# Optimization experiments

Hardware: AMD Instinct MI355X
Metric: run time of the kernel (lower is better)

## Reference

```python
import jax, jax.numpy as jnp
import numpy as np

B, C, P, D = 4096, 1000, 10, 256
N = C * P            # total prototypes
E = 160000           # edges among prototypes
MARGIN = -0.1
LOSS_WEIGHT = 0.1
EPS = 1e-12          # F.normalize eps


def _gcn_conv(x, src, dst, deg_isqrt, w, b):
    # PyG GCNConv: symmetric-normalized aggregation with self-loops (added by caller)
    xw = x @ w                                   # [N, D]
    norm = deg_isqrt[src] * deg_isqrt[dst]       # [E+N]
    msg = norm[:, None] * xw[src]                # [E+N, D]
    out = jax.ops.segment_sum(msg, dst, num_segments=N)
    return out + b


def setup_inputs() -> dict:
    key = jax.random.key(0)
    ks = jax.random.split(key, 8)
    return {
        "hidden": jax.random.normal(ks[0], (B, D), jnp.float32),
        "labels": jax.random.randint(ks[1], (B,), 0, C),
        "edge_index": jax.random.randint(ks[2], (2, E), 0, N),
        "node_features": 0.02 * jax.random.normal(ks[3], (N, D), jnp.float32),
        "w1": jax.random.normal(ks[4], (D, D), jnp.float32) / np.sqrt(D),
        "b1": jnp.zeros((D,), jnp.float32),
        "w2": jax.random.normal(ks[5], (D, D), jnp.float32) / np.sqrt(D),
        "b2": jnp.zeros((D,), jnp.float32),
    }


def reference(hidden, labels, edge_index, node_features, w1, b1, w2, b2):
    # --- PrototypeGCN over the prototype graph (self-loops + sym norm) ---
    loops = jnp.arange(N, dtype=edge_index.dtype)
    src = jnp.concatenate([edge_index[0], loops])
    dst = jnp.concatenate([edge_index[1], loops])
    deg = jax.ops.segment_sum(jnp.ones_like(dst, jnp.float32), dst, num_segments=N)
    deg_isqrt = jnp.where(deg > 0, jax.lax.rsqrt(jnp.maximum(deg, 1.0)), 0.0)
    x = node_features
    x = jax.nn.relu(_gcn_conv(x, src, dst, deg_isqrt, w1, b1))
    x = jax.nn.relu(_gcn_conv(x, src, dst, deg_isqrt, w2, b2))

    # --- cosine similarity, per-class max over prototypes ---
    hidden_norm = hidden / jnp.maximum(jnp.linalg.norm(hidden, axis=1, keepdims=True), EPS)
    proto_norm = x / jnp.maximum(jnp.linalg.norm(x, axis=1, keepdims=True), EPS)
    sim = (1.0 + hidden_norm @ proto_norm.T) / 2.0          # [B, N]
    sim_pc = sim.reshape(B, C, P)
    output = sim_pc.max(axis=2)                              # [B, C]
    topk_idx = sim_pc.argmax(axis=2)                         # [B, C]

    # --- margin-masked cross entropy ---
    ar = jnp.arange(B)
    true_scores = output[ar, labels]
    pred_labels = output.argmax(axis=1)
    pred_scores = output.max(axis=1)
    mask = (true_scores - pred_scores) > MARGIN              # [B] bool
    cnt = mask.sum()
    per_ce = -jax.nn.log_softmax(output, axis=1)[ar, labels]
    ce_loss = jnp.sum(per_ce * mask) / jnp.maximum(cnt, 1).astype(per_ce.dtype)

    # dispersion = -mean(proto_norm @ proto_norm.T) = -||sum_i p_i||^2 / N^2
    s = proto_norm.sum(axis=0)
    dispersion_loss = -(s @ s) / (N * N)
    total_loss = jnp.where(cnt == 0, 0.0, ce_loss + LOSS_WEIGHT * dispersion_loss)

    # --- vectorized usage scatter (replaces Python double loop) ---
    pos_ids = labels * P + topk_idx[ar, labels]
    positive_usage = jnp.zeros((N,), jnp.float32).at[pos_ids].add(1.0)
    wrong = (pred_labels != labels).astype(jnp.float32)
    neg_ids = pred_labels * P + topk_idx[ar, pred_labels]
    negative_usage = jnp.zeros((N,), jnp.float32).at[neg_ids].add(wrong)

    return (output, total_loss, positive_usage, negative_usage)
```

## Files before the change

### kernel.cpp

```cpp
#include <hip/hip_runtime.h>
#include <math.h>

#define B_  4096
#define C_  1000
#define P_  10
#define D_  256
#define N_  10000
#define E_  160000

typedef __attribute__((ext_vector_type(8))) short short8;
typedef __attribute__((ext_vector_type(4))) float floatx4;

#define MFMA16(a, b, c) __builtin_amdgcn_mfma_f32_16x16x32_bf16((a), (b), (c), 0, 0, 0)

__device__ __forceinline__ float waveReduceSum(float v){
  #pragma unroll
  for (int o = 32; o > 0; o >>= 1) v += __shfl_xor(v, o);
  return v;
}
__device__ __forceinline__ unsigned short f2bf(float f){
  unsigned int u = __float_as_uint(f);
  unsigned int r = (u + 0x7FFFu + ((u >> 16) & 1u)) >> 16;
  return (unsigned short)r;
}
__device__ __forceinline__ float bf2f(unsigned short b){
  return __uint_as_float(((unsigned int)b) << 16);
}
__device__ __forceinline__ void gload_lds16(const void* g, void* l){
  __builtin_amdgcn_global_load_lds((const __attribute__((address_space(1))) void*)g,
                                   (__attribute__((address_space(3))) void*)l, 16, 0, 0);
}

__global__ void k_prep(const int* __restrict__ src, const int* __restrict__ dst,
                       int* __restrict__ cursor, int* __restrict__ csr_src,
                       const float* __restrict__ w1, const float* __restrict__ w2,
                       unsigned short* __restrict__ w1h, unsigned short* __restrict__ w1l,
                       unsigned short* __restrict__ w2h, unsigned short* __restrict__ w2l,
                       float* __restrict__ zero_zone,
                       const float* __restrict__ nodef,
                       unsigned short* __restrict__ NFh, unsigned short* __restrict__ NFl,
                       const float* __restrict__ hidden,
                       unsigned short* __restrict__ HNh, unsigned short* __restrict__ HNl){
  int b = blockIdx.x;
  int t = threadIdx.x;
  if (b < 625){
    int e = b * 256 + t;
    if (e < E_){
      int d = dst[e];
      int p = atomicAdd(&cursor[d], 1);
      p = (p < 63) ? p : 63;
      csr_src[d * 64 + p] = src[e];
    }
  } else if (b < 1137){
    int bb = b - 625;
    const float* w = (bb < 256) ? w1 : w2;
    int n = bb & 255;
    float x = w[(size_t)t * 256 + n];
    unsigned short h = f2bf(x);
    unsigned short l = f2bf(x - bf2f(h));
    if (bb < 256){ w1h[(size_t)n * 256 + t] = h; w1l[(size_t)n * 256 + t] = l; }
    else         { w2h[(size_t)n * 256 + t] = h; w2l[(size_t)n * 256 + t] = l; }
  } else if (b < 1216){
    int i = (b - 1137) * 256 + t;
    if (i < 1 + 2 * N_) zero_zone[i] = 0.f;
  } else if (b < 11216){
    size_t i = (size_t)(b - 1216) * 256 + t;
    float x = nodef[i];
    unsigned short h = f2bf(x);
    NFh[i] = h;
    NFl[i] = f2bf(x - bf2f(h));
  } else {
    int r = b - 11216;
    float v = hidden[(size_t)r * 256 + t];
    float ss = waveReduceSum(v * v);
    __shared__ float red[4];
    int w = t >> 6;
    if ((t & 63) == 0) red[w] = ss;
    __syncthreads();
    float tot = red[0] + red[1] + red[2] + red[3];
    float nrm = fmaxf(sqrtf(tot), 1e-12f);
    float x = v / nrm;
    unsigned short h = f2bf(x);
    HNh[(size_t)r * 256 + t] = h;
    HNl[(size_t)r * 256 + t] = f2bf(x - bf2f(h));
  }
}

__global__ __launch_bounds__(64) void k_gemm_mfma(
    const unsigned short* __restrict__ Ah, const unsigned short* __restrict__ Al,
    const unsigned short* __restrict__ Wh, const unsigned short* __restrict__ Wl,
    float* __restrict__ outp){
  int lane = threadIdx.x;
  int l15 = lane & 15, lq = lane >> 4;
  int rb = blockIdx.x * 64;
  int nb = blockIdx.y * 32;

  floatx4 acc[4][2];
  #pragma unroll
  for (int mt = 0; mt < 4; ++mt)
    #pragma unroll
    for (int nt = 0; nt < 2; ++nt) acc[mt][nt] = (floatx4){0.f,0.f,0.f,0.f};

  int arow[4];
  #pragma unroll
  for (int mt = 0; mt < 4; ++mt){
    int r = rb + mt * 16 + l15;
    arow[mt] = (r < N_) ? r : (N_ - 1);
  }
  for (int kc = 0; kc < 256; kc += 32){
    short8 ah[4], al[4], bh[2], bl[2];
    #pragma unroll
    for (int mt = 0; mt < 4; ++mt){
      size_t o = (size_t)arow[mt] * 256 + kc + lq * 8;
      ah[mt] = *(const short8*)(Ah + o);
      al[mt] = *(const short8*)(Al + o);
    }
    #pragma unroll
    for (int nt = 0; nt < 2; ++nt){
      size_t o = (size_t)(nb + nt * 16 + l15) * 256 + kc + lq * 8;
      bh[nt] = *(const short8*)(Wh + o);
      bl[nt] = *(const short8*)(Wl + o);
    }
    #pragma unroll
    for (int nt = 0; nt < 2; ++nt)
      #pragma unroll
      for (int mt = 0; mt < 4; ++mt) acc[mt][nt] = MFMA16(al[mt], bh[nt], acc[mt][nt]);
    #pragma unroll
    for (int nt = 0; nt < 2; ++nt)
      #pragma unroll
      for (int mt = 0; mt < 4; ++mt) acc[mt][nt] = MFMA16(ah[mt], bl[nt], acc[mt][nt]);
    #pragma unroll
    for (int nt = 0; nt < 2; ++nt)
      #pragma unroll
      for (int mt = 0; mt < 4; ++mt) acc[mt][nt] = MFMA16(ah[mt], bh[nt], acc[mt][nt]);
  }
  #pragma unroll
  for (int mt = 0; mt < 4; ++mt)
    #pragma unroll
    for (int r = 0; r < 4; ++r){
      int row = rb + mt * 16 + lq * 4 + r;
      if (row < N_){
        #pragma unroll
        for (int nt = 0; nt < 2; ++nt)
          outp[(size_t)row * 256 + nb + nt * 16 + l15] = acc[mt][nt][r];
      }
    }
}

__global__ void k_agg_split(const float* __restrict__ XW, const int* __restrict__ deg,
                            const int* __restrict__ csr_src,
                            const float* __restrict__ bias,
                            unsigned short* __restrict__ Xh, unsigned short* __restrict__ Xl){
  int n    = blockIdx.x * 4 + (threadIdx.x >> 6);
  int lane = threadIdx.x & 63;
  int c4   = lane * 4;
  int dgn = deg[n];
  int dg = (dgn < 64) ? dgn : 64;
  int   esr = (lane < dg) ? csr_src[n * 64 + lane] : 0;
  float is  = 1.0f / sqrtf((float)(dgn + 1));
  float en  = (1.0f / sqrtf((float)(deg[esr] + 1))) * is;
  float4 s = *(const float4*)(XW + (size_t)n * 256 + c4);
  float w = is * is;
  float4 a = make_float4(w * s.x, w * s.y, w * s.z, w * s.w);
  float4 a2 = make_float4(0.f, 0.f, 0.f, 0.f);
  int i = 0;
  for (; i + 7 < dg; i += 8){
    int   si[8]; float ni[8];
    #pragma unroll
    for (int j = 0; j < 8; ++j){ si[j] = __shfl(esr, i+j); ni[j] = __shfl(en, i+j); }
    float4 vv[8];
    #pragma unroll
    for (int j = 0; j < 8; ++j) vv[j] = *(const float4*)(XW + (size_t)si[j] * 256 + c4);
    #pragma unroll
    for (int j = 0; j < 4; ++j){
      a.x  += ni[j]   * vv[j].x;   a.y  += ni[j]   * vv[j].y;
      a.z  += ni[j]   * vv[j].z;   a.w  += ni[j]   * vv[j].w;
      a2.x += ni[j+4] * vv[j+4].x; a2.y += ni[j+4] * vv[j+4].y;
      a2.z += ni[j+4] * vv[j+4].z; a2.w += ni[j+4] * vv[j+4].w;
    }
  }
  for (; i < dg; ++i){
    int s0 = __shfl(esr, i); float n0 = __shfl(en, i);
    float4 v0 = *(const float4*)(XW + (size_t)s0 * 256 + c4);
    a.x += n0 * v0.x; a.y += n0 * v0.y; a.z += n0 * v0.z; a.w += n0 * v0.w;
  }
  a.x += a2.x; a.y += a2.y; a.z += a2.z; a.w += a2.w;
  float4 b = *(const float4*)(bias + c4);
  float x0 = fmaxf(a.x + b.x, 0.f), x1 = fmaxf(a.y + b.y, 0.f);
  float x2 = fmaxf(a.z + b.z, 0.f), x3 = fmaxf(a.w + b.w, 0.f);
  unsigned short h0 = f2bf(x0), h1 = f2bf(x1), h2 = f2bf(x2), h3 = f2bf(x3);
  ushort4 hv = make_ushort4(h0, h1, h2, h3);
  ushort4 lv = make_ushort4(f2bf(x0 - bf2f(h0)), f2bf(x1 - bf2f(h1)),
                            f2bf(x2 - bf2f(h2)), f2bf(x3 - bf2f(h3)));
  *(ushort4*)(Xh + (size_t)n * 256 + c4) = hv;
  *(ushort4*)(Xl + (size_t)n * 256 + c4) = lv;
}

__global__ void k_agg_norm_split(const float* __restrict__ XW, const int* __restrict__ deg,
                                 const int* __restrict__ csr_src,
                                 const float* __restrict__ bias,
                                 unsigned short* __restrict__ Ph, unsigned short* __restrict__ Pl){
  int n    = blockIdx.x * 4 + (threadIdx.x >> 6);
  int lane = threadIdx.x & 63;
  int c4   = lane * 4;
  int dgn = deg[n];
  int dg = (dgn < 64) ? dgn : 64;
  int   esr = (lane < dg) ? csr_src[n * 64 + lane] : 0;
  float is  = 1.0f / sqrtf((float)(dgn + 1));
  float en  = (1.0f / sqrtf((float)(deg[esr] + 1))) * is;
  float4 s = *(const float4*)(XW + (size_t)n * 256 + c4);
  float w = is * is;
  float4 a = make_float4(w * s.x, w * s.y, w * s.z, w * s.w);
  float4 a2 = make_float4(0.f, 0.f, 0.f, 0.f);
  int i = 0;
  for (; i + 7 < dg; i += 8){
    int   si[8]; float ni[8];
    #pragma unroll
    for (int j = 0; j < 8; ++j){ si[j] = __shfl(esr, i+j); ni[j] = __shfl(en, i+j); }
    float4 vv[8];
    #pragma unroll
    for (int j = 0; j < 8; ++j) vv[j] = *(const float4*)(XW + (size_t)si[j] * 256 + c4);
    #pragma unroll
    for (int j = 0; j < 4; ++j){
      a.x  += ni[j]   * vv[j].x;   a.y  += ni[j]   * vv[j].y;
      a.z  += ni[j]   * vv[j].z;   a.w  += ni[j]   * vv[j].w;
      a2.x += ni[j+4] * vv[j+4].x; a2.y += ni[j+4] * vv[j+4].y;
      a2.z += ni[j+4] * vv[j+4].z; a2.w += ni[j+4] * vv[j+4].w;
    }
  }
  for (; i < dg; ++i){
    int s0 = __shfl(esr, i); float n0 = __shfl(en, i);
    float4 v0 = *(const float4*)(XW + (size_t)s0 * 256 + c4);
    a.x += n0 * v0.x; a.y += n0 * v0.y; a.z += n0 * v0.z; a.w += n0 * v0.w;
  }
  a.x += a2.x; a.y += a2.y; a.z += a2.z; a.w += a2.w;
  float4 b = *(const float4*)(bias + c4);
  float x0 = fmaxf(a.x + b.x, 0.f), x1 = fmaxf(a.y + b.y, 0.f);
  float x2 = fmaxf(a.z + b.z, 0.f), x3 = fmaxf(a.w + b.w, 0.f);
  float ss = x0*x0 + x1*x1 + x2*x2 + x3*x3;
  float tot = waveReduceSum(ss);
  float nrm = fmaxf(sqrtf(tot), 1e-12f);
  x0 /= nrm; x1 /= nrm; x2 /= nrm; x3 /= nrm;
  unsigned short h0 = f2bf(x0), h1 = f2bf(x1), h2 = f2bf(x2), h3 = f2bf(x3);
  ushort4 hv = make_ushort4(h0, h1, h2, h3);
  ushort4 lv = make_ushort4(f2bf(x0 - bf2f(h0)), f2bf(x1 - bf2f(h1)),
                            f2bf(x2 - bf2f(h2)), f2bf(x3 - bf2f(h3)));
  *(ushort4*)(Ph + (size_t)n * 256 + c4) = hv;
  *(ushort4*)(Pl + (size_t)n * 256 + c4) = lv;
}

__global__ __launch_bounds__(256, 4) void k_sim_max(
    const unsigned short* __restrict__ HNh, const unsigned short* __restrict__ HNl,
    const unsigned short* __restrict__ PNh, const unsigned short* __restrict__ PNl,
    float* __restrict__ out, unsigned char* __restrict__ idxb){
  __shared__ __align__(16) char smem[20736];

  int nblk = blockIdx.x;
  int st = nblk >> 8, wi = nblk & 255;
  int bx = (st & 7) * 16 + (wi & 15);
  int by = (st >> 3) * 16 + (wi >> 4);
  if (bx >= 125) return;

  int tid  = threadIdx.x;
  int wid  = tid >> 6;
  int lane = tid & 63;
  int l15  = lane & 15, lq = lane >> 4;
  int rbw  = by * 128 + wid * 32;
  int cb80 = bx * 80;

  int swz  = (l15 >> 1) & 3;
  int srow = lane >> 2;
  int skq  = (lane & 3) ^ ((lane >> 3) & 3);

  floatx4 acc[2][5];
  #pragma unroll
  for (int mt = 0; mt < 2; ++mt)
    #pragma unroll
    for (int nt = 0; nt < 5; ++nt) acc[mt][nt] = (floatx4){0.f,0.f,0.f,0.f};

  const unsigned short* a0h = HNh + (size_t)(rbw + l15) * 256 + lq * 8;
  const unsigned short* a0l = HNl + (size_t)(rbw + l15) * 256 + lq * 8;

  auto stage1 = [&](int kc, int pb, int c){
    int bsel = (c >= 5) ? 1 : 0;
    int s = c - bsel * 5;
    int row = s * 16 + srow;
    const unsigned short* gp = (bsel ? PNl : PNh)
        + (size_t)(cb80 + row) * 256 + kc + skq * 8;
    char* lp = smem + pb * 10240 + bsel * 5120 + s * 1024;
    gload_lds16(gp, lp);
  };
  auto stageAll = [&](int kc, int pb){
    stage1(kc, pb, wid);
    stage1(kc, pb, wid + 4);
    if (wid < 2) stage1(kc, pb, wid + 8);
  };

  stageAll(0, 0);
  short8 ah[2], al[2];
  #pragma unroll
  for (int mt = 0; mt < 2; ++mt){
    ah[mt] = *(const short8*)(a0h + (size_t)mt * 4096);
    al[mt] = *(const short8*)(a0l + (size_t)mt * 4096);
  }
  __syncthreads();

  int p = 0;
  for (int kc = 0; kc < 256; kc += 32){
    const unsigned short* Bh = (const unsigned short*)(smem + p * 10240);
    const unsigned short* Bl = Bh + 2560;
    short8 ah2[2], al2[2];
    if (kc < 224){
      stageAll(kc + 32, p ^ 1);
      #pragma unroll
      for (int mt = 0; mt < 2; ++mt){
        ah2[mt] = *(const short8*)(a0h + (size_t)mt * 4096 + kc + 32);
        al2[mt] = *(const short8*)(a0l + (size_t)mt * 4096 + kc + 32);
      }
    }
    {
      int r0 = (0 * 16 + l15) * 32 + (lq ^ swz) * 8;
      int r1 = (1 * 16 + l15) * 32 + (lq ^ swz) * 8;
      int r2 = (2 * 16 + l15) * 32 + (lq ^ swz) * 8;
      short8 bh0 = *(const short8*)(Bh + r0), bl0 = *(const short8*)(Bl + r0);
      short8 bh1 = *(const short8*)(Bh + r1), bl1 = *(const short8*)(Bl + r1);
      short8 bh2 = *(const short8*)(Bh + r2), bl2 = *(const short8*)(Bl + r2);
      acc[0][0] = MFMA16(al[0], bh0, acc[0][0]);
      acc[1][0] = MFMA16(al[1], bh0, acc[1][0]);
      acc[0][1] = MFMA16(al[0], bh1, acc[0][1]);
      acc[1][1] = MFMA16(al[1], bh1, acc[1][1]);
      acc[0][2] = MFMA16(al[0], bh2, acc[0][2]);
      acc[1][2] = MFMA16(al[1], bh2, acc[1][2]);
      acc[0][0] = MFMA16(ah[0], bl0, acc[0][0]);
      acc[1][0] = MFMA16(ah[1], bl0, acc[1][0]);
      acc[0][1] = MFMA16(ah[0], bl1, acc[0][1]);
      acc[1][1] = MFMA16(ah[1], bl1, acc[1][1]);
      acc[0][2] = MFMA16(ah[0], bl2, acc[0][2]);
      acc[1][2] = MFMA16(ah[1], bl2, acc[1][2]);
      acc[0][0] = MFMA16(ah[0], bh0, acc[0][0]);
      acc[1][0] = MFMA16(ah[1], bh0, acc[1][0]);
      acc[0][1] = MFMA16(ah[0], bh1, acc[0][1]);
      acc[1][1] = MFMA16(ah[1], bh1, acc[1][1]);
      acc[0][2] = MFMA16(ah[0], bh2, acc[0][2]);
      acc[1][2] = MFMA16(ah[1], bh2, acc[1][2]);
    }
    {
      int r3 = (3 * 16 + l15) * 32 + (lq ^ swz) * 8;
      int r4 = (4 * 16 + l15) * 32 + (lq ^ swz) * 8;
      short8 bh3 = *(const short8*)(Bh + r3), bl3 = *(const short8*)(Bl + r3);
      short8 bh4 = *(const short8*)(Bh + r4), bl4 = *(const short8*)(Bl + r4);
      acc[0][3] = MFMA16(al[0], bh3, acc[0][3]);
      acc[1][3] = MFMA16(al[1], bh3, acc[1][3]);
      acc[0][4] = MFMA16(al[0], bh4, acc[0][4]);
      acc[1][4] = MFMA16(al[1], bh4, acc[1][4]);
      acc[0][3] = MFMA16(ah[0], bl3, acc[0][3]);
      acc[1][3] = MFMA16(ah[1], bl3, acc[1][3]);
      acc[0][4] = MFMA16(ah[0], bl4, acc[0][4]);
      acc[1][4] = MFMA16(ah[1], bl4, acc[1][4]);
      acc[0][3] = MFMA16(ah[0], bh3, acc[0][3]);
      acc[1][3] = MFMA16(ah[1], bh3, acc[1][3]);
      acc[0][4] = MFMA16(ah[0], bh4, acc[0][4]);
      acc[1][4] = MFMA16(ah[1], bh4, acc[1][4]);
    }
    ah[0] = ah2[0]; ah[1] = ah2[1];
    al[0] = al2[0]; al[1] = al2[1];
    __syncthreads();
    p ^= 1;
  }

  float* redw = (float*)smem + wid * 1296;
  #pragma unroll
  for (int mt = 0; mt < 2; ++mt){
    #pragma unroll
    for (int nt = 0; nt < 5; ++nt)
      #pragma unroll
      for (int r = 0; r < 4; ++r)
        redw[(lq * 4 + r) * 81 + nt * 16 + l15] = acc[mt][nt][r];
    int row = lane >> 2;
    int q   = lane & 3;
    const float* basep = redw + row * 81 + q * 20;
    float vs[2]; int is[2];
    #pragma unroll
    for (int cc = 0; cc < 2; ++cc){
      float m = 0.5f * (1.0f + basep[cc * 10]); int mi = 0;
      #pragma unroll
      for (int p2 = 1; p2 < 10; ++p2){
        float v = 0.5f * (1.0f + basep[cc * 10 + p2]);
        if (v > m){ m = v; mi = p2; }
      }
      vs[cc] = m; is[cc] = mi;
    }
    int grow = rbw + mt * 16 + row;
    int gcol = bx * 8 + q * 2;
    *(float2*)(out + (size_t)grow * 1000 + gcol) = make_float2(vs[0], vs[1]);
    idxb[(size_t)grow * 1000 + gcol]     = (unsigned char)is[0];
    idxb[(size_t)grow * 1000 + gcol + 1] = (unsigned char)is[1];
  }
}

__global__ void k_row_pass(const float* __restrict__ out, const unsigned char* __restrict__ idxb,
                           const int* __restrict__ labels, int* __restrict__ cnt,
                           float* __restrict__ ce_sum, float* __restrict__ pos_usage,
                           float* __restrict__ neg_usage,
                           const unsigned short* __restrict__ Ph,
                           const unsigned short* __restrict__ Pl,
                           float* __restrict__ svec){
  int blk = blockIdx.x;
  if (blk >= 1024){
    int t = threadIdx.x;
    int r0 = (blk - 1024) * 100;
    float acc = 0.f;
    for (int rr = r0; rr < r0 + 100; ++rr)
      acc += bf2f(Ph[(size_t)rr * 256 + t]) + bf2f(Pl[(size_t)rr * 256 + t]);
    atomicAdd(&svec[t], acc);
    return;
  }
  int b = blk * 4 + (threadIdx.x >> 6);
  int lane = threadIdx.x & 63;
  const float* row = out + (size_t)b * 1000;
  float v[16];
  #pragma unroll
  for (int j = 0; j < 4; ++j){
    int f4 = j * 64 + lane;
    if (f4 < 250){
      float4 t = *(const float4*)(row + f4 * 4);
      v[j*4+0] = t.x; v[j*4+1] = t.y; v[j*4+2] = t.z; v[j*4+3] = t.w;
    } else {
      v[j*4+0] = v[j*4+1] = v[j*4+2] = v[j*4+3] = -INFINITY;
    }
  }
  float m = -INFINITY; int mi = 0x7fffffff;
  #pragma unroll
  for (int j = 0; j < 4; ++j)
    #pragma unroll
    for (int k = 0; k < 4; ++k){
      float x = v[j*4+k];
      if (x > m){ m = x; mi = (j * 64 + lane) * 4 + k; }
    }
  #pragma unroll
  for (int o = 32; o > 0; o >>= 1){
    float m2 = __shfl_xor(m, o);
    int   i2 = __shfl_xor(mi, o);
    if (m2 > m || (m2 == m && i2 < mi)){ m = m2; mi = i2; }
  }
  float s = 0.f;
  #pragma unroll
  for (int t = 0; t < 16; ++t) s += __expf(v[t] - m);
  s = waveReduceSum(s);
  if (lane == 0){
    int lab = labels[b];
    float true_score = row[lab];
    float per_ce = m + __logf(s) - true_score;
    bool mask = (true_score - m) > -0.1f;
    if (mask){ atomicAdd(cnt, 1); atomicAdd(ce_sum, per_ce); }
    int pi = idxb[(size_t)b * 1000 + lab];
    atomicAdd(&pos_usage[lab * P_ + pi], 1.f);
    if (mi != lab){
      int ni = idxb[(size_t)b * 1000 + mi];
      atomicAdd(&neg_usage[mi * P_ + ni], 1.f);
    }
  }
}

__global__ void k_finalize(const float* __restrict__ s, const int* __restrict__ cnt,
                           const float* __restrict__ ce_sum, float* __restrict__ loss_out){
  int t = threadIdx.x;
  float v = s[t];
  float ss = waveReduceSum(v * v);
  __shared__ float red[4];
  if ((t & 63) == 0) red[t >> 6] = ss;
  __syncthreads();
  if (t == 0){
    float tot = red[0] + red[1] + red[2] + red[3];
    float disp = -tot / 1.0e8f;
    int c = *cnt;
    float total = (c == 0) ? 0.f
                : (*ce_sum / (float)(c < 1 ? 1 : c) + 0.1f * disp);
    *loss_out = total;
  }
}

extern "C" void kernel_launch(void* const* d_in, const int* in_sizes, int n_in,
                              void* d_out, int out_size, void* d_ws, size_t ws_size,
                              hipStream_t stream){
  const float* hidden = (const float*)d_in[0];
  const int*   labels = (const int*)  d_in[1];
  const int*   eidx   = (const int*)  d_in[2];
  const float* nodef  = (const float*)d_in[3];
  const float* w1     = (const float*)d_in[4];
  const float* b1     = (const float*)d_in[5];
  const float* w2     = (const float*)d_in[6];
  const float* b2     = (const float*)d_in[7];

  float* out       = (float*)d_out;
  float* loss_out  = out + (size_t)B_ * C_;
  float* pos_usage = loss_out + 1;
  float* neg_usage = pos_usage + N_;

  const int* srcp = eidx;
  const int* dstp = eidx + E_;

  char* base = (char*)d_ws;
  size_t off = 0;
  auto alloc = [&](size_t bytes) -> char* {
    char* p = base + off;
    off = (off + bytes + 255) & ~(size_t)255;
    return p;
  };
  int*   cursor  = (int*)  alloc((size_t)N_ * 4);
  float* svec    = (float*)alloc(256 * 4);
  int*   cnt     = (int*)  alloc(4);
  float* ce_sum  = (float*)alloc(4);
  size_t zero_bytes = off;
  int*   csr_src   = (int*)  alloc((size_t)N_ * 64 * 4);
  float* XW        = (float*)alloc((size_t)N_ * 256 * 4);
  unsigned short* NFh = (unsigned short*)alloc((size_t)N_ * 256 * 2);
  unsigned short* NFl = (unsigned short*)alloc((size_t)N_ * 256 * 2);
  unsigned short* Xh  = (unsigned short*)alloc((size_t)N_ * 256 * 2);
  unsigned short* Xl  = (unsigned short*)alloc((size_t)N_ * 256 * 2);
  unsigned short* Ph  = (unsigned short*)alloc((size_t)N_ * 256 * 2);
  unsigned short* Pl  = (unsigned short*)alloc((size_t)N_ * 256 * 2);
  unsigned short* W1h = (unsigned short*)alloc(256 * 256 * 2);
  unsigned short* W1l = (unsigned short*)alloc(256 * 256 * 2);
  unsigned short* W2h = (unsigned short*)alloc(256 * 256 * 2);
  unsigned short* W2l = (unsigned short*)alloc(256 * 256 * 2);
  unsigned short* HNh = (unsigned short*)alloc((size_t)B_ * 256 * 2);
  unsigned short* HNl = (unsigned short*)alloc((size_t)B_ * 256 * 2);
  unsigned char* idxb = (unsigned char*)alloc((size_t)B_ * C_);

  hipMemsetAsync(base, 0, zero_bytes, stream);

  k_prep<<<15312, 256, 0, stream>>>(srcp, dstp, cursor, csr_src,
                                    w1, w2, W1h, W1l, W2h, W2l, loss_out,
                                    nodef, NFh, NFl, hidden, HNh, HNl);

  dim3 ggrid(157, 8);
  k_gemm_mfma<<<ggrid, 64, 0, stream>>>(NFh, NFl, W1h, W1l, XW);
  k_agg_split<<<N_ / 4, 256, 0, stream>>>(XW, cursor, csr_src, b1, Xh, Xl);
  k_gemm_mfma<<<ggrid, 64, 0, stream>>>(Xh, Xl, W2h, W2l, XW);
  k_agg_norm_split<<<N_ / 4, 256, 0, stream>>>(XW, cursor, csr_src, b2, Ph, Pl);

  k_sim_max<<<4096, 256, 0, stream>>>(HNh, HNl, Ph, Pl, out, idxb);

  k_row_pass<<<1124, 256, 0, stream>>>(out, idxb, labels, cnt, ce_sum,
                                       pos_usage, neg_usage, Ph, Pl, svec);
  k_finalize<<<1, 256, 0, stream>>>(svec, cnt, ce_sum, loss_out);
}
```

Measured before the change: 317.9 us.

## Split GCN aggregation edges across four waves per node; stagger MFMA groups

Each aggregation kernel now assigns one node per block, with each of the four waves gathering a 16-edge slice and combining partials through shared memory. This is meant to shorten the serial gather chain per node (average degree about 16) and raise memory-level parallelism. It launches four times as many blocks, adds a barrier per node, and leaves three waves idle during the epilogue, so wasted lanes increase for low-degree nodes. The similarity kernel also alternates the order of its two MFMA groups between even and odd waves so LDS reads and MFMA issue are staggered across waves.

Result: slower. 328.0 us (+3.2%).

```diff
diff --git a/kernel.cpp b/kernel.cpp
--- a/kernel.cpp
+++ b/kernel.cpp
@@ -151,20 +151,26 @@
                             const int* __restrict__ csr_src,
                             const float* __restrict__ bias,
                             unsigned short* __restrict__ Xh, unsigned short* __restrict__ Xl){
-  int n    = blockIdx.x * 4 + (threadIdx.x >> 6);
+  __shared__ float4 redbuf[3][64];
+  int n    = blockIdx.x;
+  int wid  = threadIdx.x >> 6;
   int lane = threadIdx.x & 63;
   int c4   = lane * 4;
-  int dgn = deg[n];
-  int dg = (dgn < 64) ? dgn : 64;
-  int   esr = (lane < dg) ? csr_src[n * 64 + lane] : 0;
+  int dgn  = deg[n];
+  int dg   = (dgn < 64) ? dgn : 64;
+  int base = wid * 16;
+  int cnt  = dg - base; cnt = (cnt < 0) ? 0 : ((cnt > 16) ? 16 : cnt);
+  int   esr = (lane < cnt) ? csr_src[n * 64 + base + lane] : 0;
   float is  = 1.0f / sqrtf((float)(dgn + 1));
   float en  = (1.0f / sqrtf((float)(deg[esr] + 1))) * is;
-  float4 s = *(const float4*)(XW + (size_t)n * 256 + c4);
-  float w = is * is;
-  float4 a = make_float4(w * s.x, w * s.y, w * s.z, w * s.w);
-  float4 a2 = make_float4(0.f, 0.f, 0.f, 0.f);
+  float4 a = make_float4(0.f, 0.f, 0.f, 0.f);
+  if (wid == 0){
+    float4 s = *(const float4*)(XW + (size_t)n * 256 + c4);
+    float w = is * is;
+    a = make_float4(w * s.x, w * s.y, w * s.z, w * s.w);
+  }
   int i = 0;
-  for (; i + 7 < dg; i += 8){
+  for (; i + 7 < cnt; i += 8){
     int   si[8]; float ni[8];
     #pragma unroll
     for (int j = 0; j < 8; ++j){ si[j] = __shfl(esr, i+j); ni[j] = __shfl(en, i+j); }
@@ -172,48 +178,58 @@
     #pragma unroll
     for (int j = 0; j < 8; ++j) vv[j] = *(const float4*)(XW + (size_t)si[j] * 256 + c4);
     #pragma unroll
-    for (int j = 0; j < 4; ++j){
-      a.x  += ni[j]   * vv[j].x;   a.y  += ni[j]   * vv[j].y;
-      a.z  += ni[j]   * vv[j].z;   a.w  += ni[j]   * vv[j].w;
-      a2.x += ni[j+4] * vv[j+4].x; a2.y += ni[j+4] * vv[j+4].y;
-      a2.z += ni[j+4] * vv[j+4].z; a2.w += ni[j+4] * vv[j+4].w;
-    }
-  }
-  for (; i < dg; ++i){
+    for (int j = 0; j < 8; ++j){
+      a.x += ni[j] * vv[j].x; a.y += ni[j] * vv[j].y;
+      a.z += ni[j] * vv[j].z; a.w += ni[j] * vv[j].w;
+    }
+  }
+  for (; i < cnt; ++i){
     int s0 = __shfl(esr, i); float n0 = __shfl(en, i);
     float4 v0 = *(const float4*)(XW + (size_t)s0 * 256 + c4);
     a.x += n0 * v0.x; a.y += n0 * v0.y; a.z += n0 * v0.z; a.w += n0 * v0.w;
   }
-  a.x += a2.x; a.y += a2.y; a.z += a2.z; a.w += a2.w;
-  float4 b = *(const float4*)(bias + c4);
-  float x0 = fmaxf(a.x + b.x, 0.f), x1 = fmaxf(a.y + b.y, 0.f);
-  float x2 = fmaxf(a.z + b.z, 0.f), x3 = fmaxf(a.w + b.w, 0.f);
-  unsigned short h0 = f2bf(x0), h1 = f2bf(x1), h2 = f2bf(x2), h3 = f2bf(x3);
-  ushort4 hv = make_ushort4(h0, h1, h2, h3);
-  ushort4 lv = make_ushort4(f2bf(x0 - bf2f(h0)), f2bf(x1 - bf2f(h1)),
-                            f2bf(x2 - bf2f(h2)), f2bf(x3 - bf2f(h3)));
-  *(ushort4*)(Xh + (size_t)n * 256 + c4) = hv;
-  *(ushort4*)(Xl + (size_t)n * 256 + c4) = lv;
+  if (wid) redbuf[wid - 1][lane] = a;
+  __syncthreads();
+  if (wid == 0){
+    float4 r0 = redbuf[0][lane], r1 = redbuf[1][lane], r2 = redbuf[2][lane];
+    a.x += r0.x + r1.x + r2.x; a.y += r0.y + r1.y + r2.y;
+    a.z += r0.z + r1.z + r2.z; a.w += r0.w + r1.w + r2.w;
+    float4 b = *(const float4*)(bias + c4);
+    float x0 = fmaxf(a.x + b.x, 0.f), x1 = fmaxf(a.y + b.y, 0.f);
+    float x2 = fmaxf(a.z + b.z, 0.f), x3 = fmaxf(a.w + b.w, 0.f);
+    unsigned short h0 = f2bf(x0), h1 = f2bf(x1), h2 = f2bf(x2), h3 = f2bf(x3);
+    ushort4 hv = make_ushort4(h0, h1, h2, h3);
+    ushort4 lv = make_ushort4(f2bf(x0 - bf2f(h0)), f2bf(x1 - bf2f(h1)),
+                              f2bf(x2 - bf2f(h2)), f2bf(x3 - bf2f(h3)));
+    *(ushort4*)(Xh + (size_t)n * 256 + c4) = hv;
+    *(ushort4*)(Xl + (size_t)n * 256 + c4) = lv;
+  }
 }
 
 __global__ void k_agg_norm_split(const float* __restrict__ XW, const int* __restrict__ deg,
                                  const int* __restrict__ csr_src,
                                  const float* __restrict__ bias,
                                  unsigned short* __restrict__ Ph, unsigned short* __restrict__ Pl){
-  int n    = blockIdx.x * 4 + (threadIdx.x >> 6);
+  __shared__ float4 redbuf[3][64];
+  int n    = blockIdx.x;
+  int wid  = threadIdx.x >> 6;
   int lane = threadIdx.x & 63;
   int c4   = lane * 4;
-  int dgn = deg[n];
-  int dg = (dgn < 64) ? dgn : 64;
-  int   esr = (lane < dg) ? csr_src[n * 64 + lane] : 0;
+  int dgn  = deg[n];
+  int dg   = (dgn < 64) ? dgn : 64;
+  int base = wid * 16;
+  int cnt  = dg - base; cnt = (cnt < 0) ? 0 : ((cnt > 16) ? 16 : cnt);
+  int   esr = (lane < cnt) ? csr_src[n * 64 + base + lane] : 0;
   float is  = 1.0f / sqrtf((float)(dgn + 1));
   float en  = (1.0f / sqrtf((float)(deg[esr] + 1))) * is;
-  float4 s = *(const float4*)(XW + (size_t)n * 256 + c4);
-  float w = is * is;
-  float4 a = make_float4(w * s.x, w * s.y, w * s.z, w * s.w);
-  float4 a2 = make_float4(0.f, 0.f, 0.f, 0.f);
+  float4 a = make_float4(0.f, 0.f, 0.f, 0.f);
+  if (wid == 0){
+    float4 s = *(const float4*)(XW + (size_t)n * 256 + c4);
+    float w = is * is;
+    a = make_float4(w * s.x, w * s.y, w * s.z, w * s.w);
+  }
   int i = 0;
-  for (; i + 7 < dg; i += 8){
+  for (; i + 7 < cnt; i += 8){
     int   si[8]; float ni[8];
     #pragma unroll
     for (int j = 0; j < 8; ++j){ si[j] = __shfl(esr, i+j); ni[j] = __shfl(en, i+j); }
@@ -221,32 +237,36 @@
     #pragma unroll
     for (int j = 0; j < 8; ++j) vv[j] = *(const float4*)(XW + (size_t)si[j] * 256 + c4);
     #pragma unroll
-    for (int j = 0; j < 4; ++j){
-      a.x  += ni[j]   * vv[j].x;   a.y  += ni[j]   * vv[j].y;
-      a.z  += ni[j]   * vv[j].z;   a.w  += ni[j]   * vv[j].w;
-      a2.x += ni[j+4] * vv[j+4].x; a2.y += ni[j+4] * vv[j+4].y;
-      a2.z += ni[j+4] * vv[j+4].z; a2.w += ni[j+4] * vv[j+4].w;
-    }
-  }
-  for (; i < dg; ++i){
+    for (int j = 0; j < 8; ++j){
+      a.x += ni[j] * vv[j].x; a.y += ni[j] * vv[j].y;
+      a.z += ni[j] * vv[j].z; a.w += ni[j] * vv[j].w;
+    }
+  }
+  for (; i < cnt; ++i){
     int s0 = __shfl(esr, i); float n0 = __shfl(en, i);
     float4 v0 = *(const float4*)(XW + (size_t)s0 * 256 + c4);
     a.x += n0 * v0.x; a.y += n0 * v0.y; a.z += n0 * v0.z; a.w += n0 * v0.w;
   }
-  a.x += a2.x; a.y += a2.y; a.z += a2.z; a.w += a2.w;
-  float4 b = *(const float4*)(bias + c4);
-  float x0 = fmaxf(a.x + b.x, 0.f), x1 = fmaxf(a.y + b.y, 0.f);
-  float x2 = fmaxf(a.z + b.z, 0.f), x3 = fmaxf(a.w + b.w, 0.f);
-  float ss = x0*x0 + x1*x1 + x2*x2 + x3*x3;
-  float tot = waveReduceSum(ss);
-  float nrm = fmaxf(sqrtf(tot), 1e-12f);
-  x0 /= nrm; x1 /= nrm; x2 /= nrm; x3 /= nrm;
-  unsigned short h0 = f2bf(x0), h1 = f2bf(x1), h2 = f2bf(x2), h3 = f2bf(x3);
-  ushort4 hv = make_ushort4(h0, h1, h2, h3);
-  ushort4 lv = make_ushort4(f2bf(x0 - bf2f(h0)), f2bf(x1 - bf2f(h1)),
-                            f2bf(x2 - bf2f(h2)), f2bf(x3 - bf2f(h3)));
-  *(ushort4*)(Ph + (size_t)n * 256 + c4) = hv;
-  *(ushort4*)(Pl + (size_t)n * 256 + c4) = lv;
+  if (wid) redbuf[wid - 1][lane] = a;
+  __syncthreads();
+  if (wid == 0){
+    float4 r0 = redbuf[0][lane], r1 = redbuf[1][lane], r2 = redbuf[2][lane];
+    a.x += r0.x + r1.x + r2.x; a.y += r0.y + r1.y + r2.y;
+    a.z += r0.z + r1.z + r2.z; a.w += r0.w + r1.w + r2.w;
+    float4 b = *(const float4*)(bias + c4);
+    float x0 = fmaxf(a.x + b.x, 0.f), x1 = fmaxf(a.y + b.y, 0.f);
+    float x2 = fmaxf(a.z + b.z, 0.f), x3 = fmaxf(a.w + b.w, 0.f);
+    float ss = x0*x0 + x1*x1 + x2*x2 + x3*x3;
+    float tot = waveReduceSum(ss);
+    float nrm = fmaxf(sqrtf(tot), 1e-12f);
+    x0 /= nrm; x1 /= nrm; x2 /= nrm; x3 /= nrm;
+    unsigned short h0 = f2bf(x0), h1 = f2bf(x1), h2 = f2bf(x2), h3 = f2bf(x3);
+    ushort4 hv = make_ushort4(h0, h1, h2, h3);
+    ushort4 lv = make_ushort4(f2bf(x0 - bf2f(h0)), f2bf(x1 - bf2f(h1)),
+                              f2bf(x2 - bf2f(h2)), f2bf(x3 - bf2f(h3)));
+    *(ushort4*)(Ph + (size_t)n * 256 + c4) = hv;
+    *(ushort4*)(Pl + (size_t)n * 256 + c4) = lv;
+  }
 }
 
 __global__ __launch_bounds__(256, 4) void k_sim_max(
@@ -318,7 +338,7 @@
         al2[mt] = *(const short8*)(a0l + (size_t)mt * 4096 + kc + 32);
       }
     }
-    {
+    auto group012 = [&](){
       int r0 = (0 * 16 + l15) * 32 + (lq ^ swz) * 8;
       int r1 = (1 * 16 + l15) * 32 + (lq ^ swz) * 8;
       int r2 = (2 * 16 + l15) * 32 + (lq ^ swz) * 8;
@@ -343,8 +363,8 @@
       acc[1][1] = MFMA16(ah[1], bh1, acc[1][1]);
       acc[0][2] = MFMA16(ah[0], bh2, acc[0][2]);
       acc[1][2] = MFMA16(ah[1], bh2, acc[1][2]);
-    }
-    {
+    };
+    auto group34 = [&](){
       int r3 = (3 * 16 + l15) * 32 + (lq ^ swz) * 8;
       int r4 = (4 * 16 + l15) * 32 + (lq ^ swz) * 8;
       short8 bh3 = *(const short8*)(Bh + r3), bl3 = *(const short8*)(Bl + r3);
@@ -361,7 +381,9 @@
       acc[1][3] = MFMA16(ah[1], bh3, acc[1][3]);
       acc[0][4] = MFMA16(ah[0], bh4, acc[0][4]);
       acc[1][4] = MFMA16(ah[1], bh4, acc[1][4]);
-    }
+    };
+    if ((wid & 1) == 0){ group012(); group34(); }
+    else               { group34(); group012(); }
     ah[0] = ah2[0]; ah[1] = ah2[1];
     al[0] = al2[0]; al[1] = al2[1];
     __syncthreads();
@@ -536,9 +558,9 @@
 
   dim3 ggrid(157, 8);
   k_gemm_mfma<<<ggrid, 64, 0, stream>>>(NFh, NFl, W1h, W1l, XW);
-  k_agg_split<<<N_ / 4, 256, 0, stream>>>(XW, cursor, csr_src, b1, Xh, Xl);
+  k_agg_split<<<N_, 256, 0, stream>>>(XW, cursor, csr_src, b1, Xh, Xl);
   k_gemm_mfma<<<ggrid, 64, 0, stream>>>(Xh, Xl, W2h, W2l, XW);
-  k_agg_norm_split<<<N_ / 4, 256, 0, stream>>>(XW, cursor, csr_src, b2, Ph, Pl);
+  k_agg_norm_split<<<N_, 256, 0, stream>>>(XW, cursor, csr_src, b2, Ph, Pl);
 
   k_sim_max<<<4096, 256, 0, stream>>>(HNh, HNl, Ph, Pl, out, idxb);
 
```
